# Kernel tuning notes

Measured on AMD Instinct MI355X. Metric: run time of the kernel, lower is better.

## Reference

```python
import jax, jax.numpy as jnp
import numpy as np

D_MODEL = 1024
N_HEADS = 16
D_KV = 64
NUM_BUCKETS = 32
MAX_DISTANCE = 128


def _relative_position_bucket(seq_len, num_buckets=NUM_BUCKETS, max_distance=MAX_DISTANCE):
    # bidirectional=True path of T5 bucketing
    ctx = jnp.arange(seq_len, dtype=jnp.int32)[:, None]
    mem = jnp.arange(seq_len, dtype=jnp.int32)[None, :]
    rel = mem - ctx  # [S, S]
    nb = num_buckets // 2
    buckets = (rel > 0).astype(jnp.int32) * nb
    rel = jnp.abs(rel)
    max_exact = nb // 2
    is_small = rel < max_exact
    # guard log(0); those entries are overridden by is_small anyway
    rel_f = jnp.maximum(rel, 1).astype(jnp.float32)
    rel_large = max_exact + (
        jnp.log(rel_f / max_exact) / np.log(max_distance / max_exact) * (nb - max_exact)
    ).astype(jnp.int32)
    rel_large = jnp.minimum(rel_large, nb - 1)
    return buckets + jnp.where(is_small, rel, rel_large)  # [S, S] int32


def setup_inputs() -> dict:
    key = jax.random.key(0)
    ks = jax.random.split(key, 11)
    B, S = 4, 2048
    hidden_states = jax.random.normal(ks[0], (B, S, D_MODEL), dtype=jnp.float32)
    attention_masks = jnp.zeros((B, 1, S, S), dtype=jnp.float32)
    w = lambda k: jax.random.normal(k, (D_MODEL, D_MODEL), dtype=jnp.float32) * 0.02
    b = lambda k: jax.random.normal(k, (D_MODEL,), dtype=jnp.float32) * 0.02
    rel_emb = jax.random.normal(ks[9], (NUM_BUCKETS, N_HEADS), dtype=jnp.float32) * 0.02
    return {
        "hidden_states": hidden_states,
        "attention_masks": attention_masks,
        "Wq": w(ks[1]), "bq": b(ks[2]),
        "Wk": w(ks[3]), "bk": b(ks[4]),
        "Wv": w(ks[5]), "bv": b(ks[6]),
        "Wo": w(ks[7]), "bo": b(ks[8]),
        "rel_emb": rel_emb,
    }


def reference(hidden_states, attention_masks, Wq, bq, Wk, bk, Wv, bv, Wo, bo, rel_emb):
    B, S, _ = hidden_states.shape

    def shape_heads(x):  # [B,S,D] -> [B,H,S,dk]
        return x.reshape(B, S, N_HEADS, D_KV).transpose(0, 2, 1, 3)

    q = shape_heads(hidden_states @ Wq.T + bq)
    k = shape_heads(hidden_states @ Wk.T + bk)
    v = shape_heads(hidden_states @ Wv.T + bv)

    scores = jnp.einsum("bhqd,bhkd->bhqk", q, k)  # [B,H,S,S]

    buckets = _relative_position_bucket(S)  # [S,S]
    position_bias = rel_emb[buckets].transpose(2, 0, 1)[None]  # [1,H,S,S]
    masks = position_bias + attention_masks  # broadcast -> [B,H,S,S]
    scores = scores + masks

    # NOTE: original scales by d_kv**2 (not sqrt), after mask addition
    attn = jax.nn.softmax(scores / float(D_KV ** 2), axis=-1)

    out = jnp.einsum("bhqk,bhkd->bhqd", attn, v)
    out = out.transpose(0, 2, 1, 3).reshape(B, S, D_MODEL)
    out = out @ Wo.T + bo
    return (out, masks)
```

## Files before the change

### kernel.cpp

```cpp
#include <hip/hip_runtime.h>
#include <cmath>


typedef __attribute__((ext_vector_type(8))) short bf16x8;
typedef __attribute__((ext_vector_type(4))) float f32x4;
typedef __attribute__((ext_vector_type(8))) unsigned short u16x8;

#define MFMA16(a, b, c) __builtin_amdgcn_mfma_f32_16x16x32_bf16((a), (b), (c), 0, 0, 0)

#define ASYNC_COPY16(g, l)                                                              \
  __builtin_amdgcn_global_load_lds((const __attribute__((address_space(1))) void*)(g),  \
                                   (__attribute__((address_space(3))) void*)(l), 16, 0, 0)

__device__ __forceinline__ unsigned short f2bf(float f) {
  unsigned u = __float_as_uint(f);
  u += 0x7FFFu + ((u >> 16) & 1u);
  return (unsigned short)(u >> 16);
}
__device__ __forceinline__ float bf2f(unsigned short u) {
  return __uint_as_float(((unsigned)u) << 16);
}

__device__ __forceinline__ int t5_bucket(int rel) {
  int bkt = (rel > 0) ? 16 : 0;
  int d = (rel < 0) ? -rel : rel;
  int v;
  if (d < 8) v = d;
  else if (d < 12) v = 8;
  else if (d < 16) v = 9;
  else if (d < 23) v = 10;
  else if (d < 32) v = 11;
  else if (d < 46) v = 12;
  else if (d < 64) v = 13;
  else if (d < 91) v = 14;
  else v = 15;
  return bkt + v;
}

struct Cast5Args {
  const float* src[5];
  unsigned short* dst[5];
};
__global__ __launch_bounds__(256) void cast5_kernel(Cast5Args a) {
  int i = (blockIdx.x * 256 + threadIdx.x) * 4;
  int seg, loc;
  if (i < 8388608) { seg = 0; loc = i; }
  else { seg = 1 + ((i - 8388608) >> 20); loc = (i - 8388608) & 1048575; }
  float4 v = *(const float4*)(a.src[seg] + loc);
  ushort4 o;
  o.x = f2bf(v.x); o.y = f2bf(v.y); o.z = f2bf(v.z); o.w = f2bf(v.w);
  *(ushort4*)(a.dst[seg] + loc) = o;
}

__device__ __forceinline__ void gemm_core(const unsigned short* __restrict__ A,
                                          const unsigned short* __restrict__ Bt,
                                          const float* __restrict__ bias,
                                          void* __restrict__ Cout, int M, int N, int K,
                                          int epi, short* sh) {
  short* As = sh;
  short* Bs = sh + 128 * 64;
  const int lane = threadIdx.x & 63;
  const int wave = threadIdx.x >> 6;
  const int l15 = lane & 15, g = lane >> 4;
  const int m0 = blockIdx.x * 128;
  const int n0 = blockIdx.y * 128;
  const int wr = wave >> 1, wc = wave & 1;

  f32x4 acc[4][4] = {};

  const int srow_in = lane >> 3;
  const int spu = lane & 7;

  for (int k0 = 0; k0 < K; k0 += 64) {
#pragma unroll
    for (int q = 0; q < 4; ++q) {
      const int rbase = (wave * 4 + q) * 8;
      const int row = rbase + srow_in;
      const int usrc = spu ^ (row & 7);
      ASYNC_COPY16(A + (size_t)(m0 + row) * K + k0 + usrc * 8, As + rbase * 64);
      ASYNC_COPY16(Bt + (size_t)(n0 + row) * K + k0 + usrc * 8, Bs + rbase * 64);
    }
    __syncthreads();

#pragma unroll
    for (int kk = 0; kk < 2; ++kk) {
      bf16x8 af[4], bfr[4];
#pragma unroll
      for (int mi = 0; mi < 4; ++mi) {
        int row = wr * 64 + mi * 16 + l15;
        int pu = (kk * 4 + g) ^ (row & 7);
        af[mi] = *(const bf16x8*)(As + row * 64 + pu * 8);
      }
#pragma unroll
      for (int ni = 0; ni < 4; ++ni) {
        int row = wc * 64 + ni * 16 + l15;
        int pu = (kk * 4 + g) ^ (row & 7);
        bfr[ni] = *(const bf16x8*)(Bs + row * 64 + pu * 8);
      }
#pragma unroll
      for (int mi = 0; mi < 4; ++mi)
#pragma unroll
        for (int ni = 0; ni < 4; ++ni)
          acc[mi][ni] = MFMA16(af[mi], bfr[ni], acc[mi][ni]);
    }
    __syncthreads();
  }

  float bvv[4];
#pragma unroll
  for (int ni = 0; ni < 4; ++ni) bvv[ni] = bias[n0 + wc * 64 + ni * 16 + l15];

  if (epi == 0) {
#pragma unroll
    for (int mi = 0; mi < 4; ++mi) {
      int rbase = m0 + wr * 64 + mi * 16 + (g << 2);
#pragma unroll
      for (int ni = 0; ni < 4; ++ni) {
        int col = n0 + wc * 64 + ni * 16 + l15;
#pragma unroll
        for (int r = 0; r < 4; ++r)
          ((float*)Cout)[(size_t)(rbase + r) * N + col] = acc[mi][ni][r] + bvv[ni];
      }
    }
  } else if (epi == 1) {
#pragma unroll
    for (int mi = 0; mi < 4; ++mi) {
      int ml = wr * 64 + mi * 16 + (g << 2);
#pragma unroll
      for (int ni = 0; ni < 4; ++ni) {
        int c = wc * 64 + ni * 16 + l15;
#pragma unroll
        for (int r = 0; r < 4; ++r) {
          int m = ml + r;
          int pc = (((c >> 3) ^ (m & 7)) << 3) | (c & 7);
          sh[m * 128 + pc] = (short)f2bf(acc[mi][ni][r] + bvv[ni]);
        }
      }
    }
    __syncthreads();
    {
      int m = threadIdx.x >> 1, half = threadIdx.x & 1;
      unsigned short* dst = (unsigned short*)Cout + (size_t)(m0 + m) * N + n0 + half * 64;
#pragma unroll
      for (int uu = 0; uu < 8; ++uu) {
        int u = half * 8 + uu;
        int pu = u ^ (m & 7);
        *(u16x8*)(dst + uu * 8) = *(const u16x8*)(sh + m * 128 + pu * 8);
      }
    }
  } else {
#pragma unroll
    for (int mi = 0; mi < 4; ++mi) {
      int ml = wr * 64 + mi * 16 + (g << 2);
#pragma unroll
      for (int ni = 0; ni < 4; ++ni) {
        int c = wc * 64 + ni * 16 + l15;
#pragma unroll
        for (int r = 0; r < 4; ++r) {
          int s = ml + r;
          int ps = (((s >> 3) ^ (c & 7)) << 3) | (s & 7);
          sh[c * 128 + ps] = (short)f2bf(acc[mi][ni][r] + bvv[ni]);
        }
      }
    }
    __syncthreads();
    {
      int c = threadIdx.x >> 1, half = threadIdx.x & 1;
      int col = n0 + c;
      int mb = m0 >> 11, ml = m0 & 2047;
      unsigned short* dst =
          (unsigned short*)Cout + (((size_t)(mb * 1024 + col)) << 11) + ml + half * 64;
#pragma unroll
      for (int uu = 0; uu < 8; ++uu) {
        int u = half * 8 + uu;
        int pu = u ^ (c & 7);
        *(u16x8*)(dst + uu * 8) = *(const u16x8*)(sh + c * 128 + pu * 8);
      }
    }
  }
}

struct QKVArgs {
  const unsigned short* A;
  const unsigned short* Bt[3];
  const float* bias[3];
  unsigned short* out[3];
};
__global__ __launch_bounds__(256) void qkv_gemm(QKVArgs a) {
  __shared__ __align__(16) short sh[2 * 128 * 64];
  const int z = blockIdx.z;
  gemm_core(a.A, a.Bt[z], a.bias[z], a.out[z], 8192, 1024, 1024, z == 2 ? 2 : 1, sh);
}

__global__ __launch_bounds__(256) void gemm_f32(const unsigned short* A,
                                                const unsigned short* Bt, const float* bias,
                                                float* Cout) {
  __shared__ __align__(16) short sh[2 * 128 * 64];
  gemm_core(A, Bt, bias, Cout, 8192, 1024, 1024, 0, sh);
}

template <int WM>
__global__ __launch_bounds__(512) void attn_fused(const unsigned short* __restrict__ Qg,
                                                  const unsigned short* __restrict__ Kg,
                                                  const unsigned short* __restrict__ Vtg,
                                                  const float* __restrict__ am,
                                                  const float* __restrict__ rel_emb,
                                                  unsigned short* __restrict__ Og,
                                                  float* __restrict__ mout) {
  const int bh = blockIdx.x;
  const int b = bh >> 4, h = bh & 15;
  const int q0 = blockIdx.y << 7;
  const int tid = threadIdx.x;
  const int lane = tid & 63, wave = tid >> 6;
  const int l15 = lane & 15, g = lane >> 4;

  __shared__ __align__(16) short Ks[64 * 72];
  __shared__ __align__(16) short Vt[64 * 72];
  __shared__ unsigned short pbr[2176];
  __shared__ __align__(16) unsigned short msPl[128 * 72];
  short* Qs = (short*)msPl;

  for (int t = tid; t < 2176; t += 512)
    pbr[t] = f2bf(rel_emb[t5_bucket(t - 127 - q0) * 16 + h]);

  const size_t base = ((size_t)b * 2048) * 1024 + h * 64;
  const size_t vtbase = (size_t)bh << 17;

  {
    int row = tid >> 2, cu = (tid & 3) << 4;
    const unsigned short* src = Qg + base + (size_t)(q0 + row) * 1024 + cu;
    u16x8 v0 = *(const u16x8*)src;
    u16x8 v1 = *(const u16x8*)(src + 8);
    *(u16x8*)(Qs + row * 72 + cu) = v0;
    *(u16x8*)(Qs + row * 72 + cu + 8) = v1;
  }
  __syncthreads();

  bf16x8 qf[2];
  {
    int row = (wave << 4) + l15;
    const short* p = Qs + row * 72 + (g << 3);
    qf[0] = *(const bf16x8*)p;
    qf[1] = *(const bf16x8*)(p + 32);
  }

  f32x4 acc[4] = {};
  f32x4 acc1 = {};
  const bf16x8 onesf = {16256, 16256, 16256, 16256, 16256, 16256, 16256, 16256};
  const int ilbase = (wave << 4) + (g << 2);
  const float SC = 1.442695041f / 4096.0f;

  const int srowK = tid >> 3;
  const int scuK = (tid & 7) << 3;
  const int mrow = tid >> 4;
  const int mf4 = tid & 15;

  for (int kt = 0; kt < 32; ++kt) {
    const int j0 = kt << 6;
    __syncthreads();
    {
      const unsigned short* ks = Kg + base + (size_t)(j0 + srowK) * 1024 + scuK;
      *(u16x8*)(Ks + srowK * 72 + scuK) = *(const u16x8*)ks;
      const unsigned short* vs = Vtg + vtbase + ((size_t)srowK << 11) + j0 + scuK;
      *(u16x8*)(Vt + srowK * 72 + scuK) = *(const u16x8*)vs;
    }
    f32x4 mreg[4];
#pragma unroll
    for (int p = 0; p < 4; ++p) {
      const int row = p * 32 + mrow;
      const int j = j0 + (mf4 << 2);
      f32x4 a = *(const f32x4*)(am + ((size_t)b * 2048 + q0 + row) * 2048 + j);
      const int pidx = j - row + 127;
      f32x4 m;
      m[0] = bf2f(pbr[pidx + 0]) + a[0];
      m[1] = bf2f(pbr[pidx + 1]) + a[1];
      m[2] = bf2f(pbr[pidx + 2]) + a[2];
      m[3] = bf2f(pbr[pidx + 3]) + a[3];
      mreg[p] = m;
      ushort4 mb;
      mb.x = f2bf(m[0]); mb.y = f2bf(m[1]); mb.z = f2bf(m[2]); mb.w = f2bf(m[3]);
      *(ushort4*)(msPl + row * 72 + (mf4 << 2)) = mb;
    }
    __syncthreads();

    if (WM) {
#pragma unroll
      for (int p = 0; p < 4; ++p) {
        const int row = p * 32 + mrow;
        f32x4* dst =
            (f32x4*)(mout + ((size_t)bh * 2048 + q0 + row) * 2048 + j0 + (mf4 << 2));
        __builtin_nontemporal_store(mreg[p], dst);
      }
    }

    f32x4 sacc[4] = {};
#pragma unroll
    for (int kk = 0; kk < 2; ++kk) {
      const int koff = (kk << 5) + (g << 3);
#pragma unroll
      for (int fj = 0; fj < 4; ++fj) {
        bf16x8 kf = *(const bf16x8*)(Ks + ((fj << 4) + l15) * 72 + koff);
        sacc[fj] = MFMA16(qf[kk], kf, sacc[fj]);
      }
    }

#pragma unroll
    for (int fj = 0; fj < 4; ++fj) {
      const int jl = (fj << 4) + l15;
#pragma unroll
      for (int r = 0; r < 4; ++r) {
        const int il = (wave << 4) + (g << 2) + r;
        float mval = bf2f(msPl[il * 72 + jl]);
        float p = exp2f((sacc[fj][r] + mval) * SC);
        msPl[il * 72 + jl] = f2bf(p);
      }
    }

#pragma unroll
    for (int kk = 0; kk < 2; ++kk) {
      const int koff = (kk << 5) + (g << 3);
      bf16x8 pf = *(const bf16x8*)((const short*)msPl + ((wave << 4) + l15) * 72 + koff);
      acc1 = MFMA16(pf, onesf, acc1);
#pragma unroll
      for (int fd = 0; fd < 4; ++fd) {
        bf16x8 vf = *(const bf16x8*)(Vt + ((fd << 4) + l15) * 72 + koff);
        acc[fd] = MFMA16(pf, vf, acc[fd]);
      }
    }
  }

#pragma unroll
  for (int fd = 0; fd < 4; ++fd) {
    int d = (fd << 4) + l15;
#pragma unroll
    for (int r = 0; r < 4; ++r) {
      float o = acc[fd][r] / acc1[r];
      Og[base + (size_t)(q0 + ilbase + r) * 1024 + d] = f2bf(o);
    }
  }
}

__global__ __launch_bounds__(256) void masks_kernel(const float* __restrict__ am,
                                                    const float* __restrict__ rel_emb,
                                                    float* __restrict__ mout) {
  const int bi = blockIdx.x;
  const int b = bi >> 11, i = bi & 2047;
  __shared__ float amrow[2048];
  __shared__ float remb[512];
  __shared__ unsigned char bkt[2048];
  for (int t = threadIdx.x; t < 512; t += 256) remb[t] = rel_emb[t];
  const float* arow = am + ((size_t)b * 2048 + i) * 2048;
  for (int t = threadIdx.x; t < 512; t += 256)
    *(float4*)(amrow + (t << 2)) = *(const float4*)(arow + (t << 2));
  for (int j = threadIdx.x; j < 2048; j += 256)
    bkt[j] = (unsigned char)t5_bucket(j - i);
  __syncthreads();
  for (int h = 0; h < 16; ++h) {
    float* dst = mout + (((size_t)(b * 16 + h)) * 2048 + i) * 2048;
    for (int t = threadIdx.x; t < 512; t += 256) {
      int j = t << 2;
      f32x4 o;
      o[0] = remb[(bkt[j + 0] << 4) + h] + amrow[j + 0];
      o[1] = remb[(bkt[j + 1] << 4) + h] + amrow[j + 1];
      o[2] = remb[(bkt[j + 2] << 4) + h] + amrow[j + 2];
      o[3] = remb[(bkt[j + 3] << 4) + h] + amrow[j + 3];
      __builtin_nontemporal_store(o, (f32x4*)(dst + j));
    }
  }
}

extern "C" void kernel_launch(void* const* d_in, const int* in_sizes, int n_in,
                              void* d_out, int out_size, void* d_ws, size_t ws_size,
                              hipStream_t stream) {
  const float* hs  = (const float*)d_in[0];
  const float* am  = (const float*)d_in[1];
  const float* Wq  = (const float*)d_in[2];
  const float* bq  = (const float*)d_in[3];
  const float* Wk  = (const float*)d_in[4];
  const float* bk  = (const float*)d_in[5];
  const float* Wv  = (const float*)d_in[6];
  const float* bv  = (const float*)d_in[7];
  const float* Wo  = (const float*)d_in[8];
  const float* bo  = (const float*)d_in[9];
  const float* rel = (const float*)d_in[10];

  float* out = (float*)d_out;
  float* mout = out + (size_t)8388608;

  const bool fused = ws_size >= (size_t)69206016;

  unsigned short *hsb, *wqb, *wkb, *wvb, *wob, *qb, *kb, *vtb, *aob;
  if (fused) {
    char* W = (char*)d_ws;
    qb  = (unsigned short*)(W);
    kb  = (unsigned short*)(W + 16777216);
    vtb = (unsigned short*)(W + 33554432);
    aob = (unsigned short*)(W + 50331648);
    wob = (unsigned short*)(W + 67108864);
    char* SB = (char*)mout;
    hsb = (unsigned short*)(SB);
    wqb = (unsigned short*)(SB + 16777216);
    wkb = (unsigned short*)(SB + 18874368);
    wvb = (unsigned short*)(SB + 20971520);
  } else {
    char* SB = (char*)mout;
    hsb = (unsigned short*)(SB);
    wqb = (unsigned short*)(SB + 16777216);
    wkb = (unsigned short*)(SB + 18874368);
    wvb = (unsigned short*)(SB + 20971520);
    wob = (unsigned short*)(SB + 23068672);
    qb  = (unsigned short*)(SB + 25165824);
    kb  = (unsigned short*)(SB + 41943040);
    vtb = (unsigned short*)(SB + 58720256);
    aob = (unsigned short*)(SB + 75497472);
  }

  Cast5Args ca;
  ca.src[0] = hs;  ca.dst[0] = hsb;
  ca.src[1] = Wq;  ca.dst[1] = wqb;
  ca.src[2] = Wk;  ca.dst[2] = wkb;
  ca.src[3] = Wv;  ca.dst[3] = wvb;
  ca.src[4] = Wo;  ca.dst[4] = wob;
  cast5_kernel<<<12288, 256, 0, stream>>>(ca);

  QKVArgs qa;
  qa.A = hsb;
  qa.Bt[0] = wqb;  qa.bias[0] = bq;  qa.out[0] = qb;
  qa.Bt[1] = wkb;  qa.bias[1] = bk;  qa.out[1] = kb;
  qa.Bt[2] = wvb;  qa.bias[2] = bv;  qa.out[2] = vtb;
  qkv_gemm<<<dim3(64, 8, 3), 256, 0, stream>>>(qa);

  if (fused) {
    attn_fused<1><<<dim3(64, 16), 512, 0, stream>>>(qb, kb, vtb, am, rel, aob, mout);
  } else {
    attn_fused<0><<<dim3(64, 16), 512, 0, stream>>>(qb, kb, vtb, am, rel, aob, mout);
  }

  gemm_f32<<<dim3(64, 8), 256, 0, stream>>>(aob, wob, bo, out);

  if (!fused) masks_kernel<<<8192, 256, 0, stream>>>(am, rel, mout);
}
```

Before: 410.5 us.

## Prefetch next K/V tile and mask into registers during attention compute

Issues the global loads for the next K and V tiles and the attention-mask slice into registers before the current tile's MFMA work, then stores them to shared memory at the next iteration. The aim is to hide global memory latency behind compute instead of stalling at the start of each iteration. It also hoists pointer arithmetic out of the loop and adds a launch-bounds occupancy hint of 6 blocks. The extra live registers could raise register pressure or cause spills under the new occupancy constraint.

```diff
diff --git a/kernel.cpp b/kernel.cpp
--- a/kernel.cpp
+++ b/kernel.cpp
@@ -200,13 +200,13 @@
 }
 
 template <int WM>
-__global__ __launch_bounds__(512) void attn_fused(const unsigned short* __restrict__ Qg,
-                                                  const unsigned short* __restrict__ Kg,
-                                                  const unsigned short* __restrict__ Vtg,
-                                                  const float* __restrict__ am,
-                                                  const float* __restrict__ rel_emb,
-                                                  unsigned short* __restrict__ Og,
-                                                  float* __restrict__ mout) {
+__global__ __launch_bounds__(512, 6) void attn_fused(const unsigned short* __restrict__ Qg,
+                                                     const unsigned short* __restrict__ Kg,
+                                                     const unsigned short* __restrict__ Vtg,
+                                                     const float* __restrict__ am,
+                                                     const float* __restrict__ rel_emb,
+                                                     unsigned short* __restrict__ Og,
+                                                     float* __restrict__ mout) {
   const int bh = blockIdx.x;
   const int b = bh >> 4, h = bh & 15;
   const int q0 = blockIdx.y << 7;
@@ -255,28 +255,39 @@
   const int mrow = tid >> 4;
   const int mf4 = tid & 15;
 
+  const unsigned short* kptr = Kg + base + (size_t)srowK * 1024 + scuK;
+  const unsigned short* vptr = Vtg + vtbase + ((size_t)srowK << 11) + scuK;
+  const float* amp[4];
+  float* mop[4];
+#pragma unroll
+  for (int p = 0; p < 4; ++p) {
+    const int row = p * 32 + mrow;
+    amp[p] = am + ((size_t)b * 2048 + q0 + row) * 2048 + (mf4 << 2);
+    mop[p] = mout + ((size_t)bh * 2048 + q0 + row) * 2048 + (mf4 << 2);
+  }
+
+  u16x8 kreg = *(const u16x8*)kptr;
+  u16x8 vreg = *(const u16x8*)vptr;
+  f32x4 amreg[4];
+#pragma unroll
+  for (int p = 0; p < 4; ++p) amreg[p] = *(const f32x4*)(amp[p]);
+
   for (int kt = 0; kt < 32; ++kt) {
     const int j0 = kt << 6;
-    __syncthreads();
-    {
-      const unsigned short* ks = Kg + base + (size_t)(j0 + srowK) * 1024 + scuK;
-      *(u16x8*)(Ks + srowK * 72 + scuK) = *(const u16x8*)ks;
-      const unsigned short* vs = Vtg + vtbase + ((size_t)srowK << 11) + j0 + scuK;
-      *(u16x8*)(Vt + srowK * 72 + scuK) = *(const u16x8*)vs;
-    }
-    f32x4 mreg[4];
+    const int j0n = (kt < 31 ? kt + 1 : 31) << 6;
+    __syncthreads();
+    *(u16x8*)(Ks + srowK * 72 + scuK) = kreg;
+    *(u16x8*)(Vt + srowK * 72 + scuK) = vreg;
 #pragma unroll
     for (int p = 0; p < 4; ++p) {
       const int row = p * 32 + mrow;
-      const int j = j0 + (mf4 << 2);
-      f32x4 a = *(const f32x4*)(am + ((size_t)b * 2048 + q0 + row) * 2048 + j);
-      const int pidx = j - row + 127;
-      f32x4 m;
-      m[0] = bf2f(pbr[pidx + 0]) + a[0];
-      m[1] = bf2f(pbr[pidx + 1]) + a[1];
-      m[2] = bf2f(pbr[pidx + 2]) + a[2];
-      m[3] = bf2f(pbr[pidx + 3]) + a[3];
-      mreg[p] = m;
+      const int pidx = j0 + (mf4 << 2) - row + 127;
+      f32x4 m = amreg[p];
+      m[0] += bf2f(pbr[pidx + 0]);
+      m[1] += bf2f(pbr[pidx + 1]);
+      m[2] += bf2f(pbr[pidx + 2]);
+      m[3] += bf2f(pbr[pidx + 3]);
+      amreg[p] = m;
       ushort4 mb;
       mb.x = f2bf(m[0]); mb.y = f2bf(m[1]); mb.z = f2bf(m[2]); mb.w = f2bf(m[3]);
       *(ushort4*)(msPl + row * 72 + (mf4 << 2)) = mb;
@@ -285,13 +296,14 @@
 
     if (WM) {
 #pragma unroll
-      for (int p = 0; p < 4; ++p) {
-        const int row = p * 32 + mrow;
-        f32x4* dst =
-            (f32x4*)(mout + ((size_t)bh * 2048 + q0 + row) * 2048 + j0 + (mf4 << 2));
-        __builtin_nontemporal_store(mreg[p], dst);
-      }
-    }
+      for (int p = 0; p < 4; ++p)
+        __builtin_nontemporal_store(amreg[p], (f32x4*)(mop[p] + j0));
+    }
+
+    kreg = *(const u16x8*)(kptr + (size_t)j0n * 1024);
+    vreg = *(const u16x8*)(vptr + j0n);
+#pragma unroll
+    for (int p = 0; p < 4; ++p) amreg[p] = *(const f32x4*)(amp[p] + j0n);
 
     f32x4 sacc[4] = {};
 #pragma unroll
```

Result: slower. 454.1 us (+10.6%).
